# Optimization experiments

Hardware: AMD Instinct MI355X
Metric: run time of the kernel (lower is better)

Reference implementation:

```python
import jax, jax.numpy as jnp
import numpy as np

INV_L_MIN, INV_L_MAX = 0.5, 2.0

def _gelu(x):
    return jax.nn.gelu(x, approximate=False)

def _scaled_sigmoid(x, lo, hi):
    return lo + (hi - lo) * jax.nn.sigmoid(x)

def _fourier_bases(nodes, modes):
    # nodes: [b, n, d]; modes: [k, d, w] -> temp: [b, n, k, w]
    temp = 2.0 * jnp.pi * jnp.einsum('bxd,kdw->bxkw', nodes, modes)
    return jnp.cos(temp), jnp.sin(temp), jnp.ones_like(temp[:, :, :1, :])

def _spectral_conv(x, wc, ws, w0, bc, bs, b0, wbc, wbs, wb0):
    # x: [b, c_in, n]; forward non-uniform Fourier transform via weighted bases
    x_c = jnp.einsum('bix,bxkw->bikw', x, wbc)
    x_s = -jnp.einsum('bix,bxkw->bikw', x, wbs)
    x_0 = jnp.einsum('bix,bxkw->bikw', x, wb0)
    f_c = jnp.einsum('bikw,iokw->bokw', x_c, wc) - jnp.einsum('bikw,iokw->bokw', x_s, ws)
    f_s = jnp.einsum('bikw,iokw->bokw', x_s, wc) + jnp.einsum('bikw,iokw->bokw', x_c, ws)
    f_0 = jnp.einsum('bikw,iokw->bokw', x_0, w0)
    return (jnp.einsum('bokw,bxkw->box', f_0, b0)
            + 2.0 * jnp.einsum('bokw,bxkw->box', f_c, bc)
            - 2.0 * jnp.einsum('bokw,bxkw->box', f_s, bs))


def setup_inputs() -> dict:
    key = jax.random.key(0)
    ks = jax.random.split(key, 32)
    B, NU, NV = 4, 65536, 16384
    K, D, W = 32, 2, 1          # nmodes, ndims, nmeasures
    C, L = 64, 3                # channels, number of BNO layers
    FC, IU, IV, OUT = 128, 2, 3, 1
    f32 = jnp.float32
    rn = lambda k, s, sc=1.0: (sc * jax.random.normal(k, s, dtype=f32))
    ru = lambda k, s, sc=1.0: (sc * jax.random.uniform(k, s, dtype=f32))
    sp_scale = 1.0 / (C * C)
    inp = {
        'u': rn(ks[0], (B, NU, IU)),
        'v': rn(ks[1], (B, NV, IV)),
        'node_mask_u': jnp.ones((B, NU, 1), dtype=jnp.int32),
        'nodes_u': ru(ks[2], (B, NU, D)),
        'nodes_v': ru(ks[3], (B, NV, D)),
        'node_weights_u': ru(ks[4], (B, NU, W), 1.0 / NU),
        'node_weights_v': ru(ks[5], (B, NV, W), 1.0 / NV),
        'modes': ru(ks[6], (K, D, W), 8.0),
        # scaled_logit(1.0, 0.5, 2.0) = log((1-0.5)/(2-1)) = log(0.5)
        'inv_L_scale_latent': jnp.full((D, W), -0.69314718, dtype=f32),
        'fc0_u_w': rn(ks[7], (C, IU), 0.5), 'fc0_u_b': rn(ks[8], (C,), 0.1),
        'fc0_v_w': rn(ks[9], (C, IV), 0.5), 'fc0_v_b': rn(ks[10], (C,), 0.1),
        'sp_ext_wc': ru(ks[11], (L, C, C, K, W), sp_scale),
        'sp_ext_ws': ru(ks[12], (L, C, C, K, W), sp_scale),
        'sp_ext_w0': ru(ks[13], (L, C, C, 1, W), sp_scale),
        'sp_u_wc': ru(ks[14], (L, C, C, K, W), sp_scale),
        'sp_u_ws': ru(ks[15], (L, C, C, K, W), sp_scale),
        'sp_u_w0': ru(ks[16], (L, C, C, 1, W), sp_scale),
        'sp_v_wc': ru(ks[17], (L, C, C, K, W), sp_scale),
        'sp_v_ws': ru(ks[18], (L, C, C, K, W), sp_scale),
        'sp_v_w0': ru(ks[19], (L, C, C, 1, W), sp_scale),
        'ws_u_w': rn(ks[20], (L, C, C), 0.05), 'ws_u_b': rn(ks[21], (L, C), 0.02),
        'ws_v_w': rn(ks[22], (L, C, C), 0.05), 'ws_v_b': rn(ks[23], (L, C), 0.02),
        'fc1_w': rn(ks[24], (FC, C), 0.05), 'fc1_b': rn(ks[25], (FC,), 0.02),
        'fc2_w': rn(ks[26], (OUT, FC), 0.05), 'fc2_b': rn(ks[27], (OUT,), 0.02),
    }
    return inp


def reference(u, v, node_mask_u, nodes_u, nodes_v, node_weights_u, node_weights_v,
              modes, inv_L_scale_latent, fc0_u_w, fc0_u_b, fc0_v_w, fc0_v_b,
              sp_ext_wc, sp_ext_ws, sp_ext_w0, sp_u_wc, sp_u_ws, sp_u_w0,
              sp_v_wc, sp_v_ws, sp_v_w0, ws_u_w, ws_u_b, ws_v_w, ws_v_b,
              fc1_w, fc1_b, fc2_w, fc2_b):
    # node_mask_u is unpacked but unused in the original forward
    m = modes * _scaled_sigmoid(inv_L_scale_latent, INV_L_MIN, INV_L_MAX)  # [k,d,w]
    bc_u, bs_u, b0_u = _fourier_bases(nodes_u, m)
    bc_v, bs_v, b0_v = _fourier_bases(nodes_v, m)
    wu = node_weights_u[:, :, None, :]  # [b,x,1,w]
    wv = node_weights_v[:, :, None, :]
    wbc_u, wbs_u, wb0_u = bc_u * wu, bs_u * wu, b0_u * wu
    wbc_v, wbs_v, wb0_v = bc_v * wv, bs_v * wv, b0_v * wv
    # lift to channel dim and move to [b, c, n]
    u = jnp.einsum('bxi,oi->box', u, fc0_u_w) + fc0_u_b[None, :, None]
    v = jnp.einsum('bxi,oi->box', v, fc0_v_w) + fc0_v_b[None, :, None]
    L = ws_u_w.shape[0]
    for i in range(L):
        u1 = _spectral_conv(v, sp_ext_wc[i], sp_ext_ws[i], sp_ext_w0[i],
                            bc_u, bs_u, b0_u, wbc_v, wbs_v, wb0_v)
        u2 = _spectral_conv(u, sp_u_wc[i], sp_u_ws[i], sp_u_w0[i],
                            bc_u, bs_u, b0_u, wbc_u, wbs_u, wb0_u)
        u3 = jnp.einsum('oi,bix->box', ws_u_w[i], u) + ws_u_b[i][None, :, None]
        u = u1 + u2 + u3
        if i != L - 1:  # v is only updated on non-final layers, as in the original
            u = _gelu(u)
            v1 = _spectral_conv(v, sp_v_wc[i], sp_v_ws[i], sp_v_w0[i],
                                bc_v, bs_v, b0_v, wbc_v, wbs_v, wb0_v)
            v2 = jnp.einsum('oi,bix->box', ws_v_w[i], v) + ws_v_b[i][None, :, None]
            v = _gelu(v1 + v2)
    u = jnp.transpose(u, (0, 2, 1))  # [b, n, c]
    u = _gelu(u @ fc1_w.T + fc1_b)
    return u @ fc2_w.T + fc2_b
```

## Files before the change

kernel.cpp:

```cpp
#include <hip/hip_runtime.h>
#include <math.h>

#define PI2 6.283185307179586f

typedef __attribute__((ext_vector_type(8))) short bf16x8;
typedef __attribute__((ext_vector_type(4))) float f32x4;

__device__ __forceinline__ float gelu_f(float x) {
    return 0.5f * x * (1.0f + erff(x * 0.7071067811865476f));
}
__device__ __forceinline__ unsigned short f2bf(float f) {
    unsigned int u = __float_as_uint(f);
    u += 0x7FFFu + ((u >> 16) & 1u);
    return (unsigned short)(u >> 16);
}
__device__ __forceinline__ float bf2f(unsigned short h) {
    return __uint_as_float(((unsigned int)h) << 16);
}
__device__ __forceinline__ unsigned int pk(unsigned short a, unsigned short b) {
    return (unsigned int)a | ((unsigned int)b << 16);
}
__device__ __forceinline__ void wsplit(float w, unsigned short* dst) {
    unsigned short h = f2bf(w);
    dst[0] = h;
    dst[128] = f2bf(w - bf2f(h));
}

template<int NIN>
__global__ __launch_bounds__(256) void k_prep(const float* __restrict__ nodes, const float* __restrict__ modes,
                                              const float* __restrict__ latent, const float* __restrict__ nw,
                                              const float* __restrict__ inp, const float* __restrict__ fcw,
                                              const float* __restrict__ fcb,
                                              unsigned short* __restrict__ FT, unsigned short* __restrict__ wbb,
                                              float* __restrict__ part, int N) {
    int b = blockIdx.y;
    int tid = threadIdx.x;
    int xl = tid & 127, half = tid >> 7;
    int x = blockIdx.x * 128 + xl;
    __shared__ unsigned short st_c[64][136];
    __shared__ unsigned short st_w[65][136];
    float s0 = 0.5f + 1.5f / (1.0f + expf(-latent[0]));
    float s1 = 0.5f + 1.5f / (1.0f + expf(-latent[1]));
    float n0 = nodes[((size_t)b * N + x) * 2 + 0];
    float n1 = nodes[((size_t)b * N + x) * 2 + 1];
    float wx = nw[(size_t)b * N + x];
    unsigned short* wb = wbb + (size_t)b * 65 * N + x;
    unsigned int fcos[8], fsin[8], fch[16];
    #pragma unroll
    for (int kk = 0; kk < 16; ++kk) {
        int k = half * 16 + kk;
        float m0 = modes[k * 2 + 0] * s0;
        float m1 = modes[k * 2 + 1] * s1;
        float t = PI2 * (n0 * m0 + n1 * m1);
        float s, c;
        sincosf(t, &s, &c);
        unsigned short hc = f2bf(c), hs = f2bf(s);
        if (kk & 1) { fcos[kk >> 1] |= ((unsigned int)hc << 16); fsin[kk >> 1] |= ((unsigned int)hs << 16); }
        else        { fcos[kk >> 1] = hc;                         fsin[kk >> 1] = hs; }
        unsigned short hcw = f2bf(c * wx), hsw = f2bf(s * wx);
        st_w[k][xl] = hcw;
        st_w[32 + k][xl] = hsw;
        wb[(size_t)k * N] = hcw;
        wb[(size_t)(32 + k) * N] = hsw;
    }
    if (half) {
        unsigned short hw = f2bf(wx);
        st_w[64][xl] = hw;
        wb[(size_t)64 * N] = hw;
    }
    float xi[NIN];
    #pragma unroll
    for (int i = 0; i < NIN; ++i) xi[i] = inp[((size_t)b * N + x) * NIN + i];
    #pragma unroll
    for (int cc = 0; cc < 32; ++cc) {
        int c = half * 32 + cc;
        float a = fcb[c];
        #pragma unroll
        for (int i = 0; i < NIN; ++i) a += fcw[c * NIN + i] * xi[i];
        unsigned short h = f2bf(a);
        st_c[c][xl] = h;
        if (cc & 1) fch[cc >> 1] |= ((unsigned int)h << 16);
        else fch[cc >> 1] = h;
    }
    unsigned int* fr = (unsigned int*)(FT + ((size_t)b * N + x) * 128);
    #pragma unroll
    for (int i = 0; i < 8; ++i) fr[half * 8 + i] = fcos[i];
    #pragma unroll
    for (int i = 0; i < 8; ++i) fr[16 + half * 8 + i] = fsin[i];
    #pragma unroll
    for (int i = 0; i < 16; ++i) fr[32 + half * 16 + i] = fch[i];
    __syncthreads();
    int lane = tid & 63, wv = tid >> 6;
    int lm = lane & 15, lg = lane >> 4;
    int ro = wv * 16;
    f32x4 acc[5] = {};
    #pragma unroll
    for (int xs = 0; xs < 128; xs += 32) {
        bf16x8 a = *(const bf16x8*)&st_c[ro + lm][xs + lg * 8];
        #pragma unroll
        for (int ct = 0; ct < 4; ++ct) {
            bf16x8 bw = *(const bf16x8*)&st_w[ct * 16 + lm][xs + lg * 8];
            acc[ct] = __builtin_amdgcn_mfma_f32_16x16x32_bf16(a, bw, acc[ct], 0, 0, 0);
        }
        bf16x8 wf = *(const bf16x8*)&st_w[64][xs + lg * 8];
        acc[4] = __builtin_amdgcn_mfma_f32_16x16x32_bf16(a, wf, acc[4], 0, 0, 0);
    }
    float* pb = part + (size_t)(b * (N / 128) + blockIdx.x) * 64 * 66;
    #pragma unroll
    for (int ct = 0; ct < 4; ++ct)
        #pragma unroll
        for (int j = 0; j < 4; ++j)
            pb[(ro + lg * 4 + j) * 66 + ct * 16 + lm] = acc[ct][j];
    if (lm == 0) {
        #pragma unroll
        for (int j = 0; j < 4; ++j) pb[(ro + lg * 4 + j) * 66 + 64] = acc[4][j];
    }
}

__global__ __launch_bounds__(256) void k_reduce2(const float* __restrict__ part_u, const float* __restrict__ part_v,
                                                 float* __restrict__ momu, float* __restrict__ momv,
                                                 int chu, int chv, int B_) {
    int by = blockIdx.y;
    const float* p;
    float* m;
    int nch, b;
    if (by < B_) { b = by; p = part_u; m = momu; nch = chu; }
    else { b = by - B_; p = part_v; m = momv; nch = chv; }
    int eg = threadIdx.x >> 3;
    int sp = threadIdx.x & 7;
    int e = blockIdx.x * 32 + eg;
    __shared__ float red[32][8];
    float s = 0.f;
    int row = 0, col = 0;
    if (e < 64 * 65) {
        row = e / 65; col = e % 65;
        const float* pp = p + ((size_t)(b * nch) * 64 + row) * 66 + col;
        for (int c = sp; c < nch; c += 8)
            s += pp[(size_t)c * 64 * 66];
    }
    red[eg][sp] = s;
    __syncthreads();
    if (sp == 0 && e < 64 * 65) {
        float t = 0.f;
        #pragma unroll
        for (int i = 0; i < 8; ++i) t += red[eg][i];
        m[((size_t)b * 64 + row) * 66 + col] = t;
    }
}

__global__ __launch_bounds__(256) void k_tw(const float* __restrict__ e_c, const float* __restrict__ e_s,
                                            const float* __restrict__ u_c, const float* __restrict__ u_s,
                                            const float* __restrict__ v_c, const float* __restrict__ v_s,
                                            float* __restrict__ oT) {
    int li = blockIdx.x;
    int a = blockIdx.y;
    const float* in;
    switch (a) {
        case 0: in = e_c; break;
        case 1: in = e_s; break;
        case 2: in = u_c; break;
        case 3: in = u_s; break;
        case 4: in = v_c; break;
        default: in = v_s; break;
    }
    float* outp = oT + (size_t)a * 393216;
    int l = li >> 6, i = li & 63;
    __shared__ float t[32][65];
    int tid = threadIdx.x;
    const float* ib = in + (size_t)l * 131072 + (size_t)i * 2048;
    #pragma unroll
    for (int r = 0; r < 8; ++r) {
        int e = r * 256 + tid;
        t[e & 31][e >> 5] = ib[e];
    }
    __syncthreads();
    float* ob = outp + (size_t)l * 131072 + (size_t)i * 64;
    #pragma unroll
    for (int r = 0; r < 8; ++r) {
        int e = r * 256 + tid;
        ob[(size_t)(e >> 6) * 4096 + (e & 63)] = t[e >> 6][e & 63];
    }
}

__global__ void k_buildW(const float* __restrict__ momu, const float* __restrict__ momv,
                         const float* __restrict__ ecT, const float* __restrict__ esT, const float* __restrict__ ew0,
                         const float* __restrict__ ucT, const float* __restrict__ usT, const float* __restrict__ uw0,
                         const float* __restrict__ vcT, const float* __restrict__ vsT, const float* __restrict__ vw0,
                         const float* __restrict__ wsuw, const float* __restrict__ wsub,
                         const float* __restrict__ wsvw, const float* __restrict__ wsvb,
                         unsigned short* __restrict__ WuBf, unsigned short* __restrict__ WvBf,
                         float* __restrict__ biasU, float* __restrict__ biasV, int do_v) {
    int b = blockIdx.y, j = blockIdx.x, o = threadIdx.x;
    const float* mu = momu + (size_t)b * 64 * 66;
    const float* mv = momv + (size_t)b * 64 * 66;
    unsigned short* Wub = WuBf + ((size_t)b * 64 + o) * 256;
    unsigned short* Wvb = WvBf + ((size_t)b * 64 + o) * 256;
    if (j < 32) {
        int k = j;
        const float* ec = ecT + (size_t)k * 4096;
        const float* es = esT + (size_t)k * 4096;
        const float* uc = ucT + (size_t)k * 4096;
        const float* us = usT + (size_t)k * 4096;
        const float* vc = vcT + (size_t)k * 4096;
        const float* vs = vsT + (size_t)k * 4096;
        float fcu = 0, fsu = 0, fcv = 0, fsv = 0;
        for (int i = 0; i < 64; ++i) {
            float Scv = mv[i * 66 + k], Ssv = mv[i * 66 + 32 + k];
            float Scu = mu[i * 66 + k], Ssu = mu[i * 66 + 32 + k];
            int wi = i * 64 + o;
            float e_c = ec[wi], e_s = es[wi];
            float u_c = uc[wi], u_s = us[wi];
            fcu += Scv * e_c + Ssv * e_s + Scu * u_c + Ssu * u_s;
            fsu += Scv * e_s - Ssv * e_c + Scu * u_s - Ssu * u_c;
            if (do_v) {
                float v_c = vc[wi], v_s = vs[wi];
                fcv += Scv * v_c + Ssv * v_s;
                fsv += Scv * v_s - Ssv * v_c;
            }
        }
        wsplit(2.f * fcu, Wub + k);
        wsplit(-2.f * fsu, Wub + 32 + k);
        if (do_v) {
            wsplit(2.f * fcv, Wvb + k);
            wsplit(-2.f * fsv, Wvb + 32 + k);
        }
    } else {
        for (int c = 0; c < 64; ++c) wsplit(wsuw[o * 64 + c], Wub + 64 + c);
        float f0u = 0;
        for (int i = 0; i < 64; ++i)
            f0u += mv[i * 66 + 64] * ew0[i * 64 + o] + mu[i * 66 + 64] * uw0[i * 64 + o];
        biasU[b * 64 + o] = f0u + wsub[o];
        if (do_v) {
            for (int c = 0; c < 64; ++c) wsplit(wsvw[o * 64 + c], Wvb + 64 + c);
            float f0v = 0;
            for (int i = 0; i < 64; ++i) f0v += mv[i * 66 + 64] * vw0[i * 64 + o];
            biasV[b * 64 + o] = f0v + wsvb[o];
        }
    }
}

__global__ void k_buildW_slow(const float* __restrict__ momu, const float* __restrict__ momv,
                              const float* __restrict__ ewc, const float* __restrict__ ews, const float* __restrict__ ew0,
                              const float* __restrict__ uwc, const float* __restrict__ uws, const float* __restrict__ uw0,
                              const float* __restrict__ vwc, const float* __restrict__ vws, const float* __restrict__ vw0,
                              const float* __restrict__ wsuw, const float* __restrict__ wsub,
                              const float* __restrict__ wsvw, const float* __restrict__ wsvb,
                              unsigned short* __restrict__ WuBf, unsigned short* __restrict__ WvBf,
                              float* __restrict__ biasU, float* __restrict__ biasV, int do_v) {
    int b = blockIdx.y, j = blockIdx.x, o = threadIdx.x;
    const float* mu = momu + (size_t)b * 64 * 66;
    const float* mv = momv + (size_t)b * 64 * 66;
    unsigned short* Wub = WuBf + ((size_t)b * 64 + o) * 256;
    unsigned short* Wvb = WvBf + ((size_t)b * 64 + o) * 256;
    if (j < 32) {
        int k = j;
        float fcu = 0, fsu = 0, fcv = 0, fsv = 0;
        for (int i = 0; i < 64; ++i) {
            float Scv = mv[i * 66 + k], Ssv = mv[i * 66 + 32 + k];
            float Scu = mu[i * 66 + k], Ssu = mu[i * 66 + 32 + k];
            int wi = (i * 64 + o) * 32 + k;
            float ec = ewc[wi], es = ews[wi];
            float uc = uwc[wi], us = uws[wi];
            fcu += Scv * ec + Ssv * es + Scu * uc + Ssu * us;
            fsu += Scv * es - Ssv * ec + Scu * us - Ssu * uc;
            if (do_v) {
                float vc = vwc[wi], vs = vws[wi];
                fcv += Scv * vc + Ssv * vs;
                fsv += Scv * vs - Ssv * vc;
            }
        }
        wsplit(2.f * fcu, Wub + k);
        wsplit(-2.f * fsu, Wub + 32 + k);
        if (do_v) {
            wsplit(2.f * fcv, Wvb + k);
            wsplit(-2.f * fsv, Wvb + 32 + k);
        }
    } else {
        for (int c = 0; c < 64; ++c) wsplit(wsuw[o * 64 + c], Wub + 64 + c);
        float f0u = 0;
        for (int i = 0; i < 64; ++i)
            f0u += mv[i * 66 + 64] * ew0[i * 64 + o] + mu[i * 66 + 64] * uw0[i * 64 + o];
        biasU[b * 64 + o] = f0u + wsub[o];
        if (do_v) {
            for (int c = 0; c < 64; ++c) wsplit(wsvw[o * 64 + c], Wvb + 64 + c);
            float f0v = 0;
            for (int i = 0; i < 64; ++i) f0v += mv[i * 66 + 64] * vw0[i * 64 + o];
            biasV[b * 64 + o] = f0v + wsvb[o];
        }
    }
}

__global__ __launch_bounds__(256) void k_synth3(const unsigned short* __restrict__ WuBf,
                                                const unsigned short* __restrict__ WvBf,
                                                const float* __restrict__ biasU, const float* __restrict__ biasV,
                                                unsigned short* FTu, unsigned short* FTv,
                                                const unsigned short* __restrict__ wbb_u,
                                                const unsigned short* __restrict__ wbb_v,
                                                float* __restrict__ part_u, float* __restrict__ part_v,
                                                int NU_, int NV_, int nbu, int act_u, int wft_v, int do_mom) {
    int bx = blockIdx.x, b = blockIdx.y, tid = threadIdx.x;
    const unsigned short* Wb;
    const float* bi;
    unsigned short* FT;
    const unsigned short* wb;
    float* pb;
    int N, act, wft, blk;
    if (bx < nbu) {
        blk = bx; Wb = WuBf; bi = biasU; FT = FTu; N = NU_;
        wb = wbb_u + (size_t)b * 65 * NU_;
        pb = part_u + (size_t)(b * (NU_ / 128) + blk) * 64 * 66;
        act = act_u; wft = 1;
    } else {
        blk = bx - nbu; Wb = WvBf; bi = biasV; FT = FTv; N = NV_;
        wb = wbb_v + (size_t)b * 65 * NV_;
        pb = part_v + (size_t)(b * (NV_ / 128) + blk) * 64 * 66;
        act = 1; wft = wft_v;
    }
    int lane = tid & 63, wv = tid >> 6;
    int lm = lane & 15, lg = lane >> 4;
    int ro = wv * 16;
    const unsigned short* Wrow = Wb + ((size_t)b * 64 + ro + lm) * 256;
    bf16x8 ahi[4], alo[4];
    #pragma unroll
    for (int kt = 0; kt < 4; ++kt) {
        ahi[kt] = *(const bf16x8*)(Wrow + kt * 32 + lg * 8);
        alo[kt] = *(const bf16x8*)(Wrow + 128 + kt * 32 + lg * 8);
    }
    float bias[4];
    #pragma unroll
    for (int j = 0; j < 4; ++j) bias[j] = bi[b * 64 + ro + lg * 4 + j];
    unsigned short* ftb = FT + (size_t)b * N * 128;
    __shared__ unsigned short st2[64][136];
    int r0 = ro + lg * 4;
    int x0 = blk * 128;
    f32x4 acc[8] = {};
    #pragma unroll
    for (int xt = 0; xt < 8; ++xt) {
        int x = x0 + xt * 16 + lm;
        const unsigned short* fp = ftb + (size_t)x * 128 + lg * 8;
        #pragma unroll
        for (int kt = 0; kt < 4; ++kt) {
            bf16x8 bf = *(const bf16x8*)(fp + kt * 32);
            acc[xt] = __builtin_amdgcn_mfma_f32_16x16x32_bf16(ahi[kt], bf, acc[xt], 0, 0, 0);
            acc[xt] = __builtin_amdgcn_mfma_f32_16x16x32_bf16(alo[kt], bf, acc[xt], 0, 0, 0);
        }
    }
    __syncthreads();
    #pragma unroll
    for (int xt = 0; xt < 8; ++xt) {
        int xl = xt * 16 + lm;
        float v[4];
        #pragma unroll
        for (int j = 0; j < 4; ++j) {
            v[j] = acc[xt][j] + bias[j];
            if (act) v[j] = gelu_f(v[j]);
        }
        unsigned short h[4];
        #pragma unroll
        for (int j = 0; j < 4; ++j) h[j] = f2bf(v[j]);
        if (do_mom) {
            st2[r0 + 0][xl] = h[0];
            st2[r0 + 1][xl] = h[1];
            st2[r0 + 2][xl] = h[2];
            st2[r0 + 3][xl] = h[3];
        }
        if (wft) {
            unsigned int* dst = (unsigned int*)(ftb + (size_t)(x0 + xl) * 128 + 64 + r0);
            dst[0] = pk(h[0], h[1]);
            dst[1] = pk(h[2], h[3]);
        }
    }
    if (do_mom) {
        __syncthreads();
        f32x4 macc[5] = {};
        #pragma unroll
        for (int xs = 0; xs < 128; xs += 32) {
            bf16x8 a = *(const bf16x8*)&st2[ro + lm][xs + lg * 8];
            #pragma unroll
            for (int ct = 0; ct < 4; ++ct) {
                bf16x8 bw = *(const bf16x8*)(wb + (size_t)(ct * 16 + lm) * N + x0 + xs + lg * 8);
                macc[ct] = __builtin_amdgcn_mfma_f32_16x16x32_bf16(a, bw, macc[ct], 0, 0, 0);
            }
            bf16x8 wf = *(const bf16x8*)(wb + (size_t)64 * N + x0 + xs + lg * 8);
            macc[4] = __builtin_amdgcn_mfma_f32_16x16x32_bf16(a, wf, macc[4], 0, 0, 0);
        }
        #pragma unroll
        for (int ct = 0; ct < 4; ++ct)
            #pragma unroll
            for (int j = 0; j < 4; ++j)
                pb[(r0 + j) * 66 + ct * 16 + lm] = macc[ct][j];
        if (lm == 0) {
            #pragma unroll
            for (int j = 0; j < 4; ++j) pb[(r0 + j) * 66 + 64] = macc[4][j];
        }
    }
}

__global__ __launch_bounds__(256) void k_fc12(const unsigned short* __restrict__ FT, const float* __restrict__ w1,
                                              const float* __restrict__ b1, const float* __restrict__ w2,
                                              const float* __restrict__ b2, float* __restrict__ out, int N) {
    int b = blockIdx.y, blk = blockIdx.x, tid = threadIdx.x;
    int lane = tid & 63, wv = tid >> 6;
    int lm = lane & 15, lg = lane >> 4;
    int f0 = wv * 32;
    bf16x8 ahi[2][2], alo[2][2];
    #pragma unroll
    for (int ft = 0; ft < 2; ++ft)
        #pragma unroll
        for (int kt = 0; kt < 2; ++kt) {
            const float* wp = w1 + (size_t)(f0 + ft * 16 + lm) * 64 + kt * 32 + lg * 8;
            float tmp[8];
            *(float4*)&tmp[0] = *(const float4*)wp;
            *(float4*)&tmp[4] = *(const float4*)(wp + 4);
            #pragma unroll
            for (int i = 0; i < 8; ++i) {
                unsigned short h = f2bf(tmp[i]);
                ahi[ft][kt][i] = (short)h;
                alo[ft][kt][i] = (short)f2bf(tmp[i] - bf2f(h));
            }
        }
    float b1v[2][4], w2v[2][4];
    #pragma unroll
    for (int ft = 0; ft < 2; ++ft)
        #pragma unroll
        for (int j = 0; j < 4; ++j) {
            int f = f0 + ft * 16 + lg * 4 + j;
            b1v[ft][j] = b1[f];
            w2v[ft][j] = w2[f];
        }
    f32x4 acc[8][2] = {};
    const unsigned short* ftb = FT + (size_t)b * N * 128;
    int x0 = blk * 128;
    #pragma unroll
    for (int xt = 0; xt < 8; ++xt) {
        const unsigned short* fp = ftb + (size_t)(x0 + xt * 16 + lm) * 128 + 64 + lg * 8;
        bf16x8 bf0 = *(const bf16x8*)fp;
        bf16x8 bf1 = *(const bf16x8*)(fp + 32);
        #pragma unroll
        for (int ft = 0; ft < 2; ++ft) {
            acc[xt][ft] = __builtin_amdgcn_mfma_f32_16x16x32_bf16(ahi[ft][0], bf0, acc[xt][ft], 0, 0, 0);
            acc[xt][ft] = __builtin_amdgcn_mfma_f32_16x16x32_bf16(alo[ft][0], bf0, acc[xt][ft], 0, 0, 0);
            acc[xt][ft] = __builtin_amdgcn_mfma_f32_16x16x32_bf16(ahi[ft][1], bf1, acc[xt][ft], 0, 0, 0);
            acc[xt][ft] = __builtin_amdgcn_mfma_f32_16x16x32_bf16(alo[ft][1], bf1, acc[xt][ft], 0, 0, 0);
        }
    }
    __shared__ float red[4][8][16];
    #pragma unroll
    for (int xt = 0; xt < 8; ++xt) {
        float s = 0.f;
        #pragma unroll
        for (int ft = 0; ft < 2; ++ft)
            #pragma unroll
            for (int j = 0; j < 4; ++j) {
                float v = acc[xt][ft][j] + b1v[ft][j];
                s += w2v[ft][j] * gelu_f(v);
            }
        s += __shfl_xor(s, 16, 64);
        s += __shfl_xor(s, 32, 64);
        if (lg == 0) red[wv][xt][lm] = s;
    }
    __syncthreads();
    if (tid < 128) {
        int xt = tid >> 4, lmm = tid & 15;
        float s = b2[0] + red[0][xt][lmm] + red[1][xt][lmm] + red[2][xt][lmm] + red[3][xt][lmm];
        out[(size_t)b * N + x0 + tid] = s;
    }
}

extern "C" void kernel_launch(void* const* d_in, const int* in_sizes, int n_in,
                              void* d_out, int out_size, void* d_ws, size_t ws_size,
                              hipStream_t stream) {
    const float* u_in = (const float*)d_in[0];
    const float* v_in = (const float*)d_in[1];
    const float* nodes_u = (const float*)d_in[3];
    const float* nodes_v = (const float*)d_in[4];
    const float* nwu = (const float*)d_in[5];
    const float* nwv = (const float*)d_in[6];
    const float* modes = (const float*)d_in[7];
    const float* latent = (const float*)d_in[8];
    const float* fc0uw = (const float*)d_in[9];
    const float* fc0ub = (const float*)d_in[10];
    const float* fc0vw = (const float*)d_in[11];
    const float* fc0vb = (const float*)d_in[12];
    const float* ewc = (const float*)d_in[13];
    const float* ews = (const float*)d_in[14];
    const float* ew0 = (const float*)d_in[15];
    const float* uwc = (const float*)d_in[16];
    const float* uws = (const float*)d_in[17];
    const float* uw0 = (const float*)d_in[18];
    const float* vwc = (const float*)d_in[19];
    const float* vws = (const float*)d_in[20];
    const float* vw0 = (const float*)d_in[21];
    const float* wsuw = (const float*)d_in[22];
    const float* wsub = (const float*)d_in[23];
    const float* wsvw = (const float*)d_in[24];
    const float* wsvb = (const float*)d_in[25];
    const float* fc1w = (const float*)d_in[26];
    const float* fc1b = (const float*)d_in[27];
    const float* fc2w = (const float*)d_in[28];
    const float* fc2b = (const float*)d_in[29];
    float* out = (float*)d_out;

    const int B = 4, NU = 65536, NV = 16384;
    const int CH_U = NU / 128, CH_V = NV / 128;

    unsigned short* FT_u = (unsigned short*)d_ws;
    unsigned short* FT_v = FT_u + (size_t)B * NU * 128;
    unsigned short* wbb_u = FT_v + (size_t)B * NV * 128;
    unsigned short* wbb_v = wbb_u + (size_t)B * 65 * NU;
    float* part_u = (float*)(wbb_v + (size_t)B * 65 * NV);
    float* part_v = part_u + (size_t)B * CH_U * 64 * 66;
    float* momu = part_v + (size_t)B * CH_V * 64 * 66;
    float* momv = momu + B * 64 * 66;
    unsigned short* WuBf = (unsigned short*)(momv + B * 64 * 66);
    unsigned short* WvBf = WuBf + (size_t)B * 64 * 256;
    float* biasU = (float*)(WvBf + (size_t)B * 64 * 256);
    float* biasV = biasU + B * 64;
    float* wT = biasV + B * 64;
    size_t need_T = (size_t)((char*)(wT + 6 * 393216) - (char*)d_ws);
    int use_T = (ws_size >= need_T) ? 1 : 0;

    k_prep<2><<<dim3(NU / 128, B), 256, 0, stream>>>(nodes_u, modes, latent, nwu, u_in, fc0uw, fc0ub,
                                                     FT_u, wbb_u, part_u, NU);
    k_prep<3><<<dim3(NV / 128, B), 256, 0, stream>>>(nodes_v, modes, latent, nwv, v_in, fc0vw, fc0vb,
                                                     FT_v, wbb_v, part_v, NV);
    if (use_T)
        k_tw<<<dim3(192, 6), 256, 0, stream>>>(ewc, ews, uwc, uws, vwc, vws, wT);

    for (int l = 0; l < 3; ++l) {
        int do_v = (l < 2) ? 1 : 0;
        k_reduce2<<<dim3(130, 2 * B), 256, 0, stream>>>(part_u, part_v, momu, momv, CH_U, CH_V, B);
        if (use_T) {
            k_buildW<<<dim3(33, B), 64, 0, stream>>>(momu, momv,
                wT + 0 * 393216 + l * 131072, wT + 1 * 393216 + l * 131072, ew0 + (size_t)l * 64 * 64,
                wT + 2 * 393216 + l * 131072, wT + 3 * 393216 + l * 131072, uw0 + (size_t)l * 64 * 64,
                wT + 4 * 393216 + l * 131072, wT + 5 * 393216 + l * 131072, vw0 + (size_t)l * 64 * 64,
                wsuw + l * 64 * 64, wsub + l * 64, wsvw + l * 64 * 64, wsvb + l * 64,
                WuBf, WvBf, biasU, biasV, do_v);
        } else {
            k_buildW_slow<<<dim3(33, B), 64, 0, stream>>>(momu, momv,
                ewc + (size_t)l * 64 * 64 * 32, ews + (size_t)l * 64 * 64 * 32, ew0 + (size_t)l * 64 * 64,
                uwc + (size_t)l * 64 * 64 * 32, uws + (size_t)l * 64 * 64 * 32, uw0 + (size_t)l * 64 * 64,
                vwc + (size_t)l * 64 * 64 * 32, vws + (size_t)l * 64 * 64 * 32, vw0 + (size_t)l * 64 * 64,
                wsuw + l * 64 * 64, wsub + l * 64, wsvw + l * 64 * 64, wsvb + l * 64,
                WuBf, WvBf, biasU, biasV, do_v);
        }
        int nbu = NU / 128;
        int nbx = nbu + (do_v ? NV / 128 : 0);
        int do_mom = (l < 2) ? 1 : 0;
        int wft_v = (l == 0) ? 1 : 0;
        k_synth3<<<dim3(nbx, B), 256, 0, stream>>>(WuBf, WvBf, biasU, biasV, FT_u, FT_v,
                                                   wbb_u, wbb_v, part_u, part_v,
                                                   NU, NV, nbu, do_v , wft_v, do_mom);
    }
    k_fc12<<<dim3(NU / 128, B), 256, 0, stream>>>(FT_u, fc1w, fc1b, fc2w, fc2b, out, NU);
}
```

Before: 482.6 us.

## Fuse final-layer synthesis with fc1/fc2 head via shared-memory staging

The last layer's synthesis kernel and the separate fc1/fc2 head kernel are merged into one kernel. The layer output is staged transposed in LDS as bf16 and fed straight into the fc1 MFMAs, so it no longer has to be written to the FT buffer in global memory and read back. The old do_mom flag is dropped from k_synth3, since that kernel now only runs for layers that need moments. This saves one launch and a global round trip of the activations, at the cost of more LDS use and register pressure in the fused kernel.

```diff
diff --git a/kernel.cpp b/kernel.cpp
--- a/kernel.cpp
+++ b/kernel.cpp
@@ -297,7 +297,7 @@
                                                 const unsigned short* __restrict__ wbb_u,
                                                 const unsigned short* __restrict__ wbb_v,
                                                 float* __restrict__ part_u, float* __restrict__ part_v,
-                                                int NU_, int NV_, int nbu, int act_u, int wft_v, int do_mom) {
+                                                int NU_, int NV_, int nbu, int act_u, int wft_v) {
     int bx = blockIdx.x, b = blockIdx.y, tid = threadIdx.x;
     const unsigned short* Wb;
     const float* bi;
@@ -358,52 +358,90 @@
         unsigned short h[4];
         #pragma unroll
         for (int j = 0; j < 4; ++j) h[j] = f2bf(v[j]);
-        if (do_mom) {
-            st2[r0 + 0][xl] = h[0];
-            st2[r0 + 1][xl] = h[1];
-            st2[r0 + 2][xl] = h[2];
-            st2[r0 + 3][xl] = h[3];
-        }
+        st2[r0 + 0][xl] = h[0];
+        st2[r0 + 1][xl] = h[1];
+        st2[r0 + 2][xl] = h[2];
+        st2[r0 + 3][xl] = h[3];
         if (wft) {
             unsigned int* dst = (unsigned int*)(ftb + (size_t)(x0 + xl) * 128 + 64 + r0);
             dst[0] = pk(h[0], h[1]);
             dst[1] = pk(h[2], h[3]);
         }
     }
-    if (do_mom) {
-        __syncthreads();
-        f32x4 macc[5] = {};
-        #pragma unroll
-        for (int xs = 0; xs < 128; xs += 32) {
-            bf16x8 a = *(const bf16x8*)&st2[ro + lm][xs + lg * 8];
-            #pragma unroll
-            for (int ct = 0; ct < 4; ++ct) {
-                bf16x8 bw = *(const bf16x8*)(wb + (size_t)(ct * 16 + lm) * N + x0 + xs + lg * 8);
-                macc[ct] = __builtin_amdgcn_mfma_f32_16x16x32_bf16(a, bw, macc[ct], 0, 0, 0);
-            }
-            bf16x8 wf = *(const bf16x8*)(wb + (size_t)64 * N + x0 + xs + lg * 8);
-            macc[4] = __builtin_amdgcn_mfma_f32_16x16x32_bf16(a, wf, macc[4], 0, 0, 0);
-        }
-        #pragma unroll
-        for (int ct = 0; ct < 4; ++ct)
-            #pragma unroll
-            for (int j = 0; j < 4; ++j)
-                pb[(r0 + j) * 66 + ct * 16 + lm] = macc[ct][j];
-        if (lm == 0) {
-            #pragma unroll
-            for (int j = 0; j < 4; ++j) pb[(r0 + j) * 66 + 64] = macc[4][j];
-        }
-    }
-}
-
-__global__ __launch_bounds__(256) void k_fc12(const unsigned short* __restrict__ FT, const float* __restrict__ w1,
-                                              const float* __restrict__ b1, const float* __restrict__ w2,
-                                              const float* __restrict__ b2, float* __restrict__ out, int N) {
-    int b = blockIdx.y, blk = blockIdx.x, tid = threadIdx.x;
+    __syncthreads();
+    f32x4 macc[5] = {};
+    #pragma unroll
+    for (int xs = 0; xs < 128; xs += 32) {
+        bf16x8 a = *(const bf16x8*)&st2[ro + lm][xs + lg * 8];
+        #pragma unroll
+        for (int ct = 0; ct < 4; ++ct) {
+            bf16x8 bw = *(const bf16x8*)(wb + (size_t)(ct * 16 + lm) * N + x0 + xs + lg * 8);
+            macc[ct] = __builtin_amdgcn_mfma_f32_16x16x32_bf16(a, bw, macc[ct], 0, 0, 0);
+        }
+        bf16x8 wf = *(const bf16x8*)(wb + (size_t)64 * N + x0 + xs + lg * 8);
+        macc[4] = __builtin_amdgcn_mfma_f32_16x16x32_bf16(a, wf, macc[4], 0, 0, 0);
+    }
+    #pragma unroll
+    for (int ct = 0; ct < 4; ++ct)
+        #pragma unroll
+        for (int j = 0; j < 4; ++j)
+            pb[(r0 + j) * 66 + ct * 16 + lm] = macc[ct][j];
+    if (lm == 0) {
+        #pragma unroll
+        for (int j = 0; j < 4; ++j) pb[(r0 + j) * 66 + 64] = macc[4][j];
+    }
+}
+
+__global__ __launch_bounds__(256) void k_synthfc(const unsigned short* __restrict__ WuBf,
+                                                 const float* __restrict__ biasU,
+                                                 const unsigned short* __restrict__ FTu,
+                                                 const float* __restrict__ w1, const float* __restrict__ b1,
+                                                 const float* __restrict__ w2, const float* __restrict__ b2,
+                                                 float* __restrict__ out, int N) {
+    int blk = blockIdx.x, b = blockIdx.y, tid = threadIdx.x;
     int lane = tid & 63, wv = tid >> 6;
     int lm = lane & 15, lg = lane >> 4;
+    int ro = wv * 16;
+    const unsigned short* Wrow = WuBf + ((size_t)b * 64 + ro + lm) * 256;
+    bf16x8 ahi[4], alo[4];
+    #pragma unroll
+    for (int kt = 0; kt < 4; ++kt) {
+        ahi[kt] = *(const bf16x8*)(Wrow + kt * 32 + lg * 8);
+        alo[kt] = *(const bf16x8*)(Wrow + 128 + kt * 32 + lg * 8);
+    }
+    float bias[4];
+    #pragma unroll
+    for (int j = 0; j < 4; ++j) bias[j] = biasU[b * 64 + ro + lg * 4 + j];
+    const unsigned short* ftb = FTu + (size_t)b * N * 128;
+    __shared__ unsigned short st2t[128][72];
+    __shared__ float red[4][8][16];
+    int r0 = ro + lg * 4;
+    int x0 = blk * 128;
+    f32x4 acc[8] = {};
+    #pragma unroll
+    for (int xt = 0; xt < 8; ++xt) {
+        int x = x0 + xt * 16 + lm;
+        const unsigned short* fp = ftb + (size_t)x * 128 + lg * 8;
+        #pragma unroll
+        for (int kt = 0; kt < 4; ++kt) {
+            bf16x8 bf = *(const bf16x8*)(fp + kt * 32);
+            acc[xt] = __builtin_amdgcn_mfma_f32_16x16x32_bf16(ahi[kt], bf, acc[xt], 0, 0, 0);
+            acc[xt] = __builtin_amdgcn_mfma_f32_16x16x32_bf16(alo[kt], bf, acc[xt], 0, 0, 0);
+        }
+    }
+    #pragma unroll
+    for (int xt = 0; xt < 8; ++xt) {
+        int xl = xt * 16 + lm;
+        float v0 = acc[xt][0] + bias[0];
+        float v1 = acc[xt][1] + bias[1];
+        float v2 = acc[xt][2] + bias[2];
+        float v3 = acc[xt][3] + bias[3];
+        *(unsigned int*)&st2t[xl][r0] = pk(f2bf(v0), f2bf(v1));
+        *(unsigned int*)&st2t[xl][r0 + 2] = pk(f2bf(v2), f2bf(v3));
+    }
+    __syncthreads();
     int f0 = wv * 32;
-    bf16x8 ahi[2][2], alo[2][2];
+    bf16x8 whi[2][2], wlo[2][2];
     #pragma unroll
     for (int ft = 0; ft < 2; ++ft)
         #pragma unroll
@@ -415,8 +453,8 @@
             #pragma unroll
             for (int i = 0; i < 8; ++i) {
                 unsigned short h = f2bf(tmp[i]);
-                ahi[ft][kt][i] = (short)h;
-                alo[ft][kt][i] = (short)f2bf(tmp[i] - bf2f(h));
+                whi[ft][kt][i] = (short)h;
+                wlo[ft][kt][i] = (short)f2bf(tmp[i] - bf2f(h));
             }
         }
     float b1v[2][4], w2v[2][4];
@@ -428,23 +466,20 @@
             b1v[ft][j] = b1[f];
             w2v[ft][j] = w2[f];
         }
-    f32x4 acc[8][2] = {};
-    const unsigned short* ftb = FT + (size_t)b * N * 128;
-    int x0 = blk * 128;
+    f32x4 facc[8][2] = {};
     #pragma unroll
     for (int xt = 0; xt < 8; ++xt) {
-        const unsigned short* fp = ftb + (size_t)(x0 + xt * 16 + lm) * 128 + 64 + lg * 8;
-        bf16x8 bf0 = *(const bf16x8*)fp;
-        bf16x8 bf1 = *(const bf16x8*)(fp + 32);
+        int xl = xt * 16 + lm;
+        bf16x8 bf0 = *(const bf16x8*)&st2t[xl][lg * 8];
+        bf16x8 bf1 = *(const bf16x8*)&st2t[xl][32 + lg * 8];
         #pragma unroll
         for (int ft = 0; ft < 2; ++ft) {
-            acc[xt][ft] = __builtin_amdgcn_mfma_f32_16x16x32_bf16(ahi[ft][0], bf0, acc[xt][ft], 0, 0, 0);
-            acc[xt][ft] = __builtin_amdgcn_mfma_f32_16x16x32_bf16(alo[ft][0], bf0, acc[xt][ft], 0, 0, 0);
-            acc[xt][ft] = __builtin_amdgcn_mfma_f32_16x16x32_bf16(ahi[ft][1], bf1, acc[xt][ft], 0, 0, 0);
-            acc[xt][ft] = __builtin_amdgcn_mfma_f32_16x16x32_bf16(alo[ft][1], bf1, acc[xt][ft], 0, 0, 0);
-        }
-    }
-    __shared__ float red[4][8][16];
+            facc[xt][ft] = __builtin_amdgcn_mfma_f32_16x16x32_bf16(whi[ft][0], bf0, facc[xt][ft], 0, 0, 0);
+            facc[xt][ft] = __builtin_amdgcn_mfma_f32_16x16x32_bf16(wlo[ft][0], bf0, facc[xt][ft], 0, 0, 0);
+            facc[xt][ft] = __builtin_amdgcn_mfma_f32_16x16x32_bf16(whi[ft][1], bf1, facc[xt][ft], 0, 0, 0);
+            facc[xt][ft] = __builtin_amdgcn_mfma_f32_16x16x32_bf16(wlo[ft][1], bf1, facc[xt][ft], 0, 0, 0);
+        }
+    }
     #pragma unroll
     for (int xt = 0; xt < 8; ++xt) {
         float s = 0.f;
@@ -452,7 +487,7 @@
         for (int ft = 0; ft < 2; ++ft)
             #pragma unroll
             for (int j = 0; j < 4; ++j) {
-                float v = acc[xt][ft][j] + b1v[ft][j];
+                float v = facc[xt][ft][j] + b1v[ft][j];
                 s += w2v[ft][j] * gelu_f(v);
             }
         s += __shfl_xor(s, 16, 64);
@@ -545,13 +580,16 @@
                 wsuw + l * 64 * 64, wsub + l * 64, wsvw + l * 64 * 64, wsvb + l * 64,
                 WuBf, WvBf, biasU, biasV, do_v);
         }
-        int nbu = NU / 128;
-        int nbx = nbu + (do_v ? NV / 128 : 0);
-        int do_mom = (l < 2) ? 1 : 0;
-        int wft_v = (l == 0) ? 1 : 0;
-        k_synth3<<<dim3(nbx, B), 256, 0, stream>>>(WuBf, WvBf, biasU, biasV, FT_u, FT_v,
-                                                   wbb_u, wbb_v, part_u, part_v,
-                                                   NU, NV, nbu, do_v , wft_v, do_mom);
-    }
-    k_fc12<<<dim3(NU / 128, B), 256, 0, stream>>>(FT_u, fc1w, fc1b, fc2w, fc2b, out, NU);
-}
+        if (l < 2) {
+            int nbu = NU / 128;
+            int nbx = nbu + NV / 128;
+            int wft_v = (l == 0) ? 1 : 0;
+            k_synth3<<<dim3(nbx, B), 256, 0, stream>>>(WuBf, WvBf, biasU, biasV, FT_u, FT_v,
+                                                       wbb_u, wbb_v, part_u, part_v,
+                                                       NU, NV, nbu, 1 , wft_v);
+        } else {
+            k_synthfc<<<dim3(NU / 128, B), 256, 0, stream>>>(WuBf, biasU, FT_u,
+                                                             fc1w, fc1b, fc2w, fc2b, out, NU);
+        }
+    }
+}
```

After: 465.1 us. 3.6% less time.
